# Kernel optimization log

Hardware: AMD Instinct MI355X
Metric: run time of the kernel (lower is better)

## Reference

```python
import jax, jax.numpy as jnp
import numpy as np

T, B, I, H, NCLS = 1024, 256, 128, 128, 18

def setup_inputs() -> dict:
    key = jax.random.key(0)
    ks = jax.random.split(key, 8)
    s = 1.0 / np.sqrt(H)  # torch nn.LSTM/Linear init bound
    inp = jax.random.normal(ks[0], (T, B, I), dtype=jnp.float32)
    hidden = jnp.zeros((1, B, H), dtype=jnp.float32)
    cell = jnp.zeros((1, B, H), dtype=jnp.float32)
    W_ih = jax.random.uniform(ks[1], (4 * H, I), jnp.float32, -s, s)
    W_hh = jax.random.uniform(ks[2], (4 * H, H), jnp.float32, -s, s)
    b_ih = jax.random.uniform(ks[3], (4 * H,), jnp.float32, -s, s)
    b_hh = jax.random.uniform(ks[4], (4 * H,), jnp.float32, -s, s)
    fc_W = jax.random.uniform(ks[5], (NCLS, H), jnp.float32, -s, s)
    fc_b = jax.random.uniform(ks[6], (NCLS,), jnp.float32, -s, s)
    return {"input": inp, "hidden": hidden, "cell": cell, "W_ih": W_ih,
            "W_hh": W_hh, "b_ih": b_ih, "b_hh": b_hh, "fc_W": fc_W, "fc_b": fc_b}

def reference(input, hidden, cell, W_ih, W_hh, b_ih, b_hh, fc_W, fc_b):
    # Single-layer unidirectional LSTM (PyTorch gate order i,f,g,o) + Linear head.
    h0, c0 = hidden[0], cell[0]  # [B,H]
    b = b_ih + b_hh

    def step(carry, x_t):
        h, c = carry
        gates = x_t @ W_ih.T + h @ W_hh.T + b  # [B,4H]
        i, f, g, o = jnp.split(gates, 4, axis=-1)
        i = jax.nn.sigmoid(i)
        f = jax.nn.sigmoid(f)
        g = jnp.tanh(g)
        o = jax.nn.sigmoid(o)
        c = f * c + i * g
        h = o * jnp.tanh(c)
        return (h, c), h

    (hT, cT), hs = jax.lax.scan(step, (h0, c0), input)  # hs: [T,B,H]
    out = hs @ fc_W.T + fc_b  # [T,B,18]
    return (out, (hT[None], cT[None]))
```

## Files before the change

### kernel.cpp

```cpp
#include <hip/hip_runtime.h>
#include <cstdint>
#include <cstddef>

#define TSTEPS 1024
#define NB 256
#define NI 128
#define NH 128
#define NC 18
#define CH 32
#define NCHUNK (TSTEPS/CH)
#define XGS 516

#define LOG2E_F     1.44269504088896f
#define TWO_LOG2E_F 2.88539008177793f

typedef _Float16 f16x8 __attribute__((ext_vector_type(8)));
typedef float    f32x4 __attribute__((ext_vector_type(4)));
typedef _Float16 half2_t __attribute__((ext_vector_type(2)));

__device__ __forceinline__ half2_t as_h2(uint32_t v){
  union { uint32_t u; half2_t h; } cv; cv.u = v; return cv.h;
}
__device__ __forceinline__ uint32_t pku(float a, float b){
  union { half2_t h; uint32_t u; } cv; cv.h.x=(_Float16)a; cv.h.y=(_Float16)b; return cv.u;
}
__device__ __forceinline__ float dot2f(half2_t a, half2_t b, float c){
#if __has_builtin(__builtin_amdgcn_fdot2)
  return __builtin_amdgcn_fdot2(a, b, c, false);
#else
  return c + (float)a.x*(float)b.x + (float)a.y*(float)b.y;
#endif
}
__device__ __forceinline__ float fast_rcp(float x){
#if __has_builtin(__builtin_amdgcn_rcpf)
  return __builtin_amdgcn_rcpf(x);
#else
  return 1.f / x;
#endif
}
__device__ __forceinline__ float exp2x(float v){
#if __has_builtin(__builtin_amdgcn_exp2f)
  return __builtin_amdgcn_exp2f(v);
#else
  return __expf(v * 0.6931471805599453f);
#endif
}
template<int CTRL>
__device__ __forceinline__ float qbcast(float v){
#if __has_builtin(__builtin_amdgcn_mov_dpp)
  union { float f; int i; } u; u.f = v;
  u.i = __builtin_amdgcn_mov_dpp(u.i, CTRL, 0xF, 0xF, false);
  return u.f;
#else
  return __shfl(v, ((threadIdx.x & 63) & ~3) + (CTRL & 3), 64);
#endif
}
__device__ __forceinline__ f16x8 ldrow_f16s(const float* base, float s){
  float4 f0 = ((const float4*)base)[0];
  float4 f1 = ((const float4*)base)[1];
  f16x8 r;
  r[0]=(_Float16)(f0.x*s); r[1]=(_Float16)(f0.y*s); r[2]=(_Float16)(f0.z*s); r[3]=(_Float16)(f0.w*s);
  r[4]=(_Float16)(f1.x*s); r[5]=(_Float16)(f1.y*s); r[6]=(_Float16)(f1.z*s); r[7]=(_Float16)(f1.w*s);
  return r;
}
__device__ __forceinline__ void barrier_lds(){
  asm volatile("s_waitcnt lgkmcnt(0)" ::: "memory");
  __builtin_amdgcn_s_barrier();
}

__global__ __launch_bounds__(512, 2) void lstm_mfma(
    const float* __restrict__ x,
    const float* __restrict__ h0,
    const float* __restrict__ c0,
    const float* __restrict__ Wih,
    const float* __restrict__ Whh,
    const float* __restrict__ bih,
    const float* __restrict__ bhh,
    const float* __restrict__ fcW,
    const float* __restrict__ fcb,
    float* __restrict__ out,
    float* __restrict__ hT,
    float* __restrict__ cT)
{
  const int b    = blockIdx.x;
  const int tid  = threadIdx.x;
  const int w    = tid >> 6;
  const int l    = tid & 63;
  const int n    = l & 15;
  const int quad = l >> 4;
  const int q4   = l & 3;
  const int c4   = (l >> 2) & 3;

  __shared__ __align__(16) _Float16 xs[CH][136];
  __shared__ __align__(16) float    xgp[CH][XGS];
  __shared__ __align__(16) _Float16 hist[CH][128];
  __shared__ __align__(16) uint32_t fcw[NC][66];

  const float sc = (q4 == 2) ? TWO_LOG2E_F : LOG2E_F;
  f16x8 whh[4][4], wih[4][4];
  float biasv[4];
#pragma unroll
  for (int m = 0; m < 4; ++m){
    const int row = q4*128 + w*16 + 4*m + c4;
#pragma unroll
    for (int kt = 0; kt < 4; ++kt){
      whh[m][kt] = ldrow_f16s(Whh + (size_t)row*NH + kt*32 + quad*8, sc);
      wih[m][kt] = ldrow_f16s(Wih + (size_t)row*NI + kt*32 + quad*8, sc);
    }
    biasv[m] = (bih[row] + bhh[row]) * sc;
  }

  const uint32_t smask = (q4 == 2) ? 0u : 0x80000000u;
  const float aK = (q4 == 2) ? 1.f : 0.f;
  const float sK = (q4 == 2) ? -2.f : 1.f;

  const int mycell = w*16 + quad*4 + c4;
  float cst = c0[(size_t)b*NH + mycell];
  float hlast = 0.f;

  if (tid < 128) hist[CH-1][tid] = (_Float16)h0[(size_t)b*NH + tid];
#pragma unroll
  for (int r = 0; r < 3; ++r){
    int idx = tid + 512*r;
    if (idx < NC*64){
      int j = idx >> 6, k = idx & 63;
      float2 f = ((const float2*)(fcW + (size_t)j*NH))[k];
      fcw[j][k] = pku(f.x, f.y);
    }
  }

  const int ttA = tid >> 5;
  const int ttB = ttA + 16;
  const int k4  = tid & 31;
  float4 xpA = ((const float4*)(x + ((size_t)ttA*NB + b)*NI))[k4];
  float4 xpB = ((const float4*)(x + ((size_t)ttB*NB + b)*NI))[k4];
  __syncthreads();

#pragma unroll 1
  for (int ck = 0; ck < NCHUNK; ++ck){
    const int t0 = ck*CH;

    {
      union { _Float16 h[4]; uint2 u2; } pa, pb;
      pa.h[0]=(_Float16)xpA.x; pa.h[1]=(_Float16)xpA.y;
      pa.h[2]=(_Float16)xpA.z; pa.h[3]=(_Float16)xpA.w;
      *(uint2*)&xs[ttA][4*k4] = pa.u2;
      pb.h[0]=(_Float16)xpB.x; pb.h[1]=(_Float16)xpB.y;
      pb.h[2]=(_Float16)xpB.z; pb.h[3]=(_Float16)xpB.w;
      *(uint2*)&xs[ttB][4*k4] = pb.u2;
    }
    barrier_lds();

    {
      f16x8 xa[2][4];
#pragma unroll
      for (int mt = 0; mt < 2; ++mt)
#pragma unroll
        for (int kt = 0; kt < 4; ++kt)
          xa[mt][kt] = *(const f16x8*)&xs[mt*16 + n][kt*32 + quad*8];

#pragma unroll
      for (int m = 0; m < 4; ++m){
#pragma unroll
        for (int mt = 0; mt < 2; ++mt){
          f32x4 acc = { biasv[m], biasv[m], biasv[m], biasv[m] };
#pragma unroll
          for (int kt = 0; kt < 4; ++kt)
            acc = __builtin_amdgcn_mfma_f32_16x16x32_f16(xa[mt][kt], wih[m][kt], acc, 0, 0, 0);
#pragma unroll
          for (int r = 0; r < 4; ++r)
            xgp[mt*16 + quad*4 + r][w*64 + n*4 + m] = acc[r];
        }
      }
    }

    if (ck + 1 < NCHUNK){
      const size_t t1 = (size_t)(t0 + CH);
      xpA = ((const float4*)(x + ((t1 + ttA)*NB + b)*NI))[k4];
      xpB = ((const float4*)(x + ((t1 + ttB)*NB + b)*NI))[k4];
    }
    barrier_lds();

#pragma unroll 4
    for (int tt = 0; tt < CH; ++tt){
      f32x4 sgv = *(const f32x4*)&xgp[tt][w*64 + n*4];
      const int rp = (tt + CH - 1) & (CH - 1);
      const _Float16* hprev = &hist[rp][0];
      f16x8 a0 = *(const f16x8*)&hprev[ 0 + quad*8];
      f16x8 a1 = *(const f16x8*)&hprev[32 + quad*8];
      f16x8 a2 = *(const f16x8*)&hprev[64 + quad*8];
      f16x8 a3 = *(const f16x8*)&hprev[96 + quad*8];
      float g0, g1, g2, g3;
      {
        f32x4 aA, aB;
        aA[0] = sgv[0];
        aA = __builtin_amdgcn_mfma_f32_16x16x32_f16(a0, whh[0][0], aA, 0, 0, 0);
        aA = __builtin_amdgcn_mfma_f32_16x16x32_f16(a1, whh[0][1], aA, 0, 0, 0);
        aB[0] = 0.f;
        aB = __builtin_amdgcn_mfma_f32_16x16x32_f16(a2, whh[0][2], aB, 0, 0, 0);
        aB = __builtin_amdgcn_mfma_f32_16x16x32_f16(a3, whh[0][3], aB, 0, 0, 0);
        g0 = aA[0] + aB[0];
      }
      {
        f32x4 aA, aB;
        aA[0] = sgv[1];
        aA = __builtin_amdgcn_mfma_f32_16x16x32_f16(a0, whh[1][0], aA, 0, 0, 0);
        aA = __builtin_amdgcn_mfma_f32_16x16x32_f16(a1, whh[1][1], aA, 0, 0, 0);
        aB[0] = 0.f;
        aB = __builtin_amdgcn_mfma_f32_16x16x32_f16(a2, whh[1][2], aB, 0, 0, 0);
        aB = __builtin_amdgcn_mfma_f32_16x16x32_f16(a3, whh[1][3], aB, 0, 0, 0);
        g1 = aA[0] + aB[0];
      }
      {
        f32x4 aA, aB;
        aA[0] = sgv[2];
        aA = __builtin_amdgcn_mfma_f32_16x16x32_f16(a0, whh[2][0], aA, 0, 0, 0);
        aA = __builtin_amdgcn_mfma_f32_16x16x32_f16(a1, whh[2][1], aA, 0, 0, 0);
        aB[0] = 0.f;
        aB = __builtin_amdgcn_mfma_f32_16x16x32_f16(a2, whh[2][2], aB, 0, 0, 0);
        aB = __builtin_amdgcn_mfma_f32_16x16x32_f16(a3, whh[2][3], aB, 0, 0, 0);
        g2 = aA[0] + aB[0];
      }
      {
        f32x4 aA, aB;
        aA[0] = sgv[3];
        aA = __builtin_amdgcn_mfma_f32_16x16x32_f16(a0, whh[3][0], aA, 0, 0, 0);
        aA = __builtin_amdgcn_mfma_f32_16x16x32_f16(a1, whh[3][1], aA, 0, 0, 0);
        aB[0] = 0.f;
        aB = __builtin_amdgcn_mfma_f32_16x16x32_f16(a2, whh[3][2], aB, 0, 0, 0);
        aB = __builtin_amdgcn_mfma_f32_16x16x32_f16(a3, whh[3][3], aB, 0, 0, 0);
        g3 = aA[0] + aB[0];
      }
      const bool qlo = (quad & 1) != 0;
      const bool qhi = (quad & 2) != 0;
      float gsel = qhi ? (qlo ? g3 : g2) : (qlo ? g1 : g0);
      union { float f; uint32_t u; } gx; gx.f = gsel; gx.u ^= smask;
      float ev  = exp2x(gx.f);
      float rr  = fast_rcp(1.f + ev);
      float act = __builtin_fmaf(sK, rr, aK);
      float vi = qbcast<0x00>(act);
      float vf = qbcast<0x55>(act);
      float vg = qbcast<0xAA>(act);
      float vo = qbcast<0xFF>(act);
      cst = __builtin_fmaf(vf, cst, vi*vg);
      float e2 = exp2x(cst * TWO_LOG2E_F);
      float tc = __builtin_fmaf(-2.f, fast_rcp(1.f + e2), 1.f);
      float hv = vo * tc;
      hlast = hv;
      if (q4 == 0)
        hist[tt][mycell] = (_Float16)hv;
      barrier_lds();
    }

    {
      const int tt = tid >> 4;
      const int jb = tid & 15;
      const uint4* hb = (const uint4*)&hist[tt][0];
#pragma unroll
      for (int jj = 0; jj < 2; ++jj){
        const int j = jj*16 + jb;
        if (j < NC){
          const uint2* fw = (const uint2*)&fcw[j][0];
          float a0=0.f, a1=0.f, a2=0.f, a3=0.f;
#pragma unroll
          for (int q = 0; q < 4; ++q){
            uint4 v0 = hb[q], v1 = hb[4+q], v2 = hb[8+q], v3 = hb[12+q];
            uint2 f0a = fw[2*q],    f0b = fw[2*q+1];
            uint2 f1a = fw[8+2*q],  f1b = fw[8+2*q+1];
            uint2 f2a = fw[16+2*q], f2b = fw[16+2*q+1];
            uint2 f3a = fw[24+2*q], f3b = fw[24+2*q+1];
            a0 = dot2f(as_h2(f0a.x), as_h2(v0.x), a0);
            a1 = dot2f(as_h2(f1a.x), as_h2(v1.x), a1);
            a2 = dot2f(as_h2(f2a.x), as_h2(v2.x), a2);
            a3 = dot2f(as_h2(f3a.x), as_h2(v3.x), a3);
            a0 = dot2f(as_h2(f0a.y), as_h2(v0.y), a0);
            a1 = dot2f(as_h2(f1a.y), as_h2(v1.y), a1);
            a2 = dot2f(as_h2(f2a.y), as_h2(v2.y), a2);
            a3 = dot2f(as_h2(f3a.y), as_h2(v3.y), a3);
            a0 = dot2f(as_h2(f0b.x), as_h2(v0.z), a0);
            a1 = dot2f(as_h2(f1b.x), as_h2(v1.z), a1);
            a2 = dot2f(as_h2(f2b.x), as_h2(v2.z), a2);
            a3 = dot2f(as_h2(f3b.x), as_h2(v3.z), a3);
            a0 = dot2f(as_h2(f0b.y), as_h2(v0.w), a0);
            a1 = dot2f(as_h2(f1b.y), as_h2(v1.w), a1);
            a2 = dot2f(as_h2(f2b.y), as_h2(v2.w), a2);
            a3 = dot2f(as_h2(f3b.y), as_h2(v3.w), a3);
          }
          out[(size_t)(t0+tt)*NB*NC + (size_t)b*NC + j] =
              (a0+a1) + (a2+a3) + fcb[j];
        }
      }
    }
  }

  if (q4 == 0){
    hT[(size_t)b*NH + mycell] = hlast;
    cT[(size_t)b*NH + mycell] = cst;
  }
}

extern "C" void kernel_launch(void* const* d_in, const int* in_sizes, int n_in,
                              void* d_out, int out_size, void* d_ws, size_t ws_size,
                              hipStream_t stream) {
  (void)in_sizes; (void)n_in; (void)d_ws; (void)ws_size; (void)out_size;
  const float* x   = (const float*)d_in[0];
  const float* h0  = (const float*)d_in[1];
  const float* c0  = (const float*)d_in[2];
  const float* Wih = (const float*)d_in[3];
  const float* Whh = (const float*)d_in[4];
  const float* bih = (const float*)d_in[5];
  const float* bhh = (const float*)d_in[6];
  const float* fcW = (const float*)d_in[7];
  const float* fcb = (const float*)d_in[8];
  float* out = (float*)d_out;
  float* hT  = out + (size_t)TSTEPS*NB*NC;
  float* cT  = hT + (size_t)NB*NH;
  hipLaunchKernelGGL(lstm_mfma, dim3(NB), dim3(512), 0, stream,
                     x, h0, c0, Wih, Whh, bih, bhh, fcW, fcb, out, hT, cT);
}
```

Before: 723.4 us.

## Halve LSTM block to 256 threads with two hidden cells per lane

The kernel now uses 4 waves of 256 threads instead of 8, and each wave owns 32 hidden cells instead of 16. Each lane therefore keeps twice as many W_hh/W_ih fragments in registers, issues 8 gate MFMA groups per step and updates two cells, with a packed half2 write into the history. The aim is cheaper per-timestep barriers and more MFMA work in flight per wave on the serial recurrence. In exchange register pressure doubles, which risks spills at one block per CU. The loader and FC-head work are remapped to fit the smaller block.

```diff
diff --git a/kernel.cpp b/kernel.cpp
--- a/kernel.cpp
+++ b/kernel.cpp
@@ -68,7 +68,7 @@
   __builtin_amdgcn_s_barrier();
 }
 
-__global__ __launch_bounds__(512, 2) void lstm_mfma(
+__global__ __launch_bounds__(256, 1) void lstm_mfma(
     const float* __restrict__ x,
     const float* __restrict__ h0,
     const float* __restrict__ c0,
@@ -97,11 +97,11 @@
   __shared__ __align__(16) uint32_t fcw[NC][66];
 
   const float sc = (q4 == 2) ? TWO_LOG2E_F : LOG2E_F;
-  f16x8 whh[4][4], wih[4][4];
-  float biasv[4];
-#pragma unroll
-  for (int m = 0; m < 4; ++m){
-    const int row = q4*128 + w*16 + 4*m + c4;
+  f16x8 whh[8][4], wih[8][4];
+  float biasv[8];
+#pragma unroll
+  for (int m = 0; m < 8; ++m){
+    const int row = q4*128 + w*32 + (m&3)*8 + (n>>2)*2 + (m>>2);
 #pragma unroll
     for (int kt = 0; kt < 4; ++kt){
       whh[m][kt] = ldrow_f16s(Whh + (size_t)row*NH + kt*32 + quad*8, sc);
@@ -114,14 +114,15 @@
   const float aK = (q4 == 2) ? 1.f : 0.f;
   const float sK = (q4 == 2) ? -2.f : 1.f;
 
-  const int mycell = w*16 + quad*4 + c4;
-  float cst = c0[(size_t)b*NH + mycell];
-  float hlast = 0.f;
+  const int cellA = w*32 + quad*8 + c4*2;
+  float cstA = c0[(size_t)b*NH + cellA];
+  float cstB = c0[(size_t)b*NH + cellA + 1];
+  float hlastA = 0.f, hlastB = 0.f;
 
   if (tid < 128) hist[CH-1][tid] = (_Float16)h0[(size_t)b*NH + tid];
 #pragma unroll
-  for (int r = 0; r < 3; ++r){
-    int idx = tid + 512*r;
+  for (int r = 0; r < 5; ++r){
+    int idx = tid + 256*r;
     if (idx < NC*64){
       int j = idx >> 6, k = idx & 63;
       float2 f = ((const float2*)(fcW + (size_t)j*NH))[k];
@@ -129,11 +130,18 @@
     }
   }
 
-  const int ttA = tid >> 5;
-  const int ttB = ttA + 16;
-  const int k4  = tid & 31;
-  float4 xpA = ((const float4*)(x + ((size_t)ttA*NB + b)*NI))[k4];
-  float4 xpB = ((const float4*)(x + ((size_t)ttB*NB + b)*NI))[k4];
+  const int hrow = tid >> 3;
+  const int hj   = tid & 7;
+  const float fj0 = fcb[hj];
+  const float fj1 = fcb[hj + 8];
+  const float fj2 = (hj < 2) ? fcb[16 + hj] : 0.f;
+
+  const int srow = tid >> 3;
+  const int sc8  = tid & 7;
+  float4 xp0 = ((const float4*)(x + ((size_t)srow*NB + b)*NI))[sc8];
+  float4 xp1 = ((const float4*)(x + ((size_t)srow*NB + b)*NI))[sc8 + 8];
+  float4 xp2 = ((const float4*)(x + ((size_t)srow*NB + b)*NI))[sc8 + 16];
+  float4 xp3 = ((const float4*)(x + ((size_t)srow*NB + b)*NI))[sc8 + 24];
   __syncthreads();
 
 #pragma unroll 1
@@ -141,13 +149,15 @@
     const int t0 = ck*CH;
 
     {
-      union { _Float16 h[4]; uint2 u2; } pa, pb;
-      pa.h[0]=(_Float16)xpA.x; pa.h[1]=(_Float16)xpA.y;
-      pa.h[2]=(_Float16)xpA.z; pa.h[3]=(_Float16)xpA.w;
-      *(uint2*)&xs[ttA][4*k4] = pa.u2;
-      pb.h[0]=(_Float16)xpB.x; pb.h[1]=(_Float16)xpB.y;
-      pb.h[2]=(_Float16)xpB.z; pb.h[3]=(_Float16)xpB.w;
-      *(uint2*)&xs[ttB][4*k4] = pb.u2;
+      union { _Float16 h[4]; uint2 u2; } p0, p1, p2, p3;
+      p0.h[0]=(_Float16)xp0.x; p0.h[1]=(_Float16)xp0.y; p0.h[2]=(_Float16)xp0.z; p0.h[3]=(_Float16)xp0.w;
+      p1.h[0]=(_Float16)xp1.x; p1.h[1]=(_Float16)xp1.y; p1.h[2]=(_Float16)xp1.z; p1.h[3]=(_Float16)xp1.w;
+      p2.h[0]=(_Float16)xp2.x; p2.h[1]=(_Float16)xp2.y; p2.h[2]=(_Float16)xp2.z; p2.h[3]=(_Float16)xp2.w;
+      p3.h[0]=(_Float16)xp3.x; p3.h[1]=(_Float16)xp3.y; p3.h[2]=(_Float16)xp3.z; p3.h[3]=(_Float16)xp3.w;
+      *(uint2*)&xs[srow][4*sc8]        = p0.u2;
+      *(uint2*)&xs[srow][4*(sc8 + 8)]  = p1.u2;
+      *(uint2*)&xs[srow][4*(sc8 + 16)] = p2.u2;
+      *(uint2*)&xs[srow][4*(sc8 + 24)] = p3.u2;
     }
     barrier_lds();
 
@@ -160,7 +170,7 @@
           xa[mt][kt] = *(const f16x8*)&xs[mt*16 + n][kt*32 + quad*8];
 
 #pragma unroll
-      for (int m = 0; m < 4; ++m){
+      for (int m = 0; m < 8; ++m){
 #pragma unroll
         for (int mt = 0; mt < 2; ++mt){
           f32x4 acc = { biasv[m], biasv[m], biasv[m], biasv[m] };
@@ -169,133 +179,106 @@
             acc = __builtin_amdgcn_mfma_f32_16x16x32_f16(xa[mt][kt], wih[m][kt], acc, 0, 0, 0);
 #pragma unroll
           for (int r = 0; r < 4; ++r)
-            xgp[mt*16 + quad*4 + r][w*64 + n*4 + m] = acc[r];
+            xgp[mt*16 + quad*4 + r][w*128 + n*8 + m] = acc[r];
         }
       }
     }
 
     if (ck + 1 < NCHUNK){
       const size_t t1 = (size_t)(t0 + CH);
-      xpA = ((const float4*)(x + ((t1 + ttA)*NB + b)*NI))[k4];
-      xpB = ((const float4*)(x + ((t1 + ttB)*NB + b)*NI))[k4];
+      xp0 = ((const float4*)(x + ((t1 + srow)*NB + b)*NI))[sc8];
+      xp1 = ((const float4*)(x + ((t1 + srow)*NB + b)*NI))[sc8 + 8];
+      xp2 = ((const float4*)(x + ((t1 + srow)*NB + b)*NI))[sc8 + 16];
+      xp3 = ((const float4*)(x + ((t1 + srow)*NB + b)*NI))[sc8 + 24];
     }
     barrier_lds();
 
-#pragma unroll 4
+#pragma unroll 2
     for (int tt = 0; tt < CH; ++tt){
-      f32x4 sgv = *(const f32x4*)&xgp[tt][w*64 + n*4];
+      f32x4 s0 = *(const f32x4*)&xgp[tt][w*128 + n*8];
+      f32x4 s1 = *(const f32x4*)&xgp[tt][w*128 + n*8 + 4];
       const int rp = (tt + CH - 1) & (CH - 1);
       const _Float16* hprev = &hist[rp][0];
       f16x8 a0 = *(const f16x8*)&hprev[ 0 + quad*8];
       f16x8 a1 = *(const f16x8*)&hprev[32 + quad*8];
       f16x8 a2 = *(const f16x8*)&hprev[64 + quad*8];
       f16x8 a3 = *(const f16x8*)&hprev[96 + quad*8];
-      float g0, g1, g2, g3;
-      {
+      float g[8];
+#pragma unroll
+      for (int m = 0; m < 4; ++m){
         f32x4 aA, aB;
-        aA[0] = sgv[0];
-        aA = __builtin_amdgcn_mfma_f32_16x16x32_f16(a0, whh[0][0], aA, 0, 0, 0);
-        aA = __builtin_amdgcn_mfma_f32_16x16x32_f16(a1, whh[0][1], aA, 0, 0, 0);
+        aA[0] = s0[m];
+        aA = __builtin_amdgcn_mfma_f32_16x16x32_f16(a0, whh[m][0], aA, 0, 0, 0);
+        aA = __builtin_amdgcn_mfma_f32_16x16x32_f16(a1, whh[m][1], aA, 0, 0, 0);
         aB[0] = 0.f;
-        aB = __builtin_amdgcn_mfma_f32_16x16x32_f16(a2, whh[0][2], aB, 0, 0, 0);
-        aB = __builtin_amdgcn_mfma_f32_16x16x32_f16(a3, whh[0][3], aB, 0, 0, 0);
-        g0 = aA[0] + aB[0];
+        aB = __builtin_amdgcn_mfma_f32_16x16x32_f16(a2, whh[m][2], aB, 0, 0, 0);
+        aB = __builtin_amdgcn_mfma_f32_16x16x32_f16(a3, whh[m][3], aB, 0, 0, 0);
+        g[m] = aA[0] + aB[0];
       }
-      {
+#pragma unroll
+      for (int m = 0; m < 4; ++m){
         f32x4 aA, aB;
-        aA[0] = sgv[1];
-        aA = __builtin_amdgcn_mfma_f32_16x16x32_f16(a0, whh[1][0], aA, 0, 0, 0);
-        aA = __builtin_amdgcn_mfma_f32_16x16x32_f16(a1, whh[1][1], aA, 0, 0, 0);
+        aA[0] = s1[m];
+        aA = __builtin_amdgcn_mfma_f32_16x16x32_f16(a0, whh[4+m][0], aA, 0, 0, 0);
+        aA = __builtin_amdgcn_mfma_f32_16x16x32_f16(a1, whh[4+m][1], aA, 0, 0, 0);
         aB[0] = 0.f;
-        aB = __builtin_amdgcn_mfma_f32_16x16x32_f16(a2, whh[1][2], aB, 0, 0, 0);
-        aB = __builtin_amdgcn_mfma_f32_16x16x32_f16(a3, whh[1][3], aB, 0, 0, 0);
-        g1 = aA[0] + aB[0];
-      }
-      {
-        f32x4 aA, aB;
-        aA[0] = sgv[2];
-        aA = __builtin_amdgcn_mfma_f32_16x16x32_f16(a0, whh[2][0], aA, 0, 0, 0);
-        aA = __builtin_amdgcn_mfma_f32_16x16x32_f16(a1, whh[2][1], aA, 0, 0, 0);
-        aB[0] = 0.f;
-        aB = __builtin_amdgcn_mfma_f32_16x16x32_f16(a2, whh[2][2], aB, 0, 0, 0);
-        aB = __builtin_amdgcn_mfma_f32_16x16x32_f16(a3, whh[2][3], aB, 0, 0, 0);
-        g2 = aA[0] + aB[0];
-      }
-      {
-        f32x4 aA, aB;
-        aA[0] = sgv[3];
-        aA = __builtin_amdgcn_mfma_f32_16x16x32_f16(a0, whh[3][0], aA, 0, 0, 0);
-        aA = __builtin_amdgcn_mfma_f32_16x16x32_f16(a1, whh[3][1], aA, 0, 0, 0);
-        aB[0] = 0.f;
-        aB = __builtin_amdgcn_mfma_f32_16x16x32_f16(a2, whh[3][2], aB, 0, 0, 0);
-        aB = __builtin_amdgcn_mfma_f32_16x16x32_f16(a3, whh[3][3], aB, 0, 0, 0);
-        g3 = aA[0] + aB[0];
+        aB = __builtin_amdgcn_mfma_f32_16x16x32_f16(a2, whh[4+m][2], aB, 0, 0, 0);
+        aB = __builtin_amdgcn_mfma_f32_16x16x32_f16(a3, whh[4+m][3], aB, 0, 0, 0);
+        g[4+m] = aA[0] + aB[0];
       }
       const bool qlo = (quad & 1) != 0;
       const bool qhi = (quad & 2) != 0;
-      float gsel = qhi ? (qlo ? g3 : g2) : (qlo ? g1 : g0);
-      union { float f; uint32_t u; } gx; gx.f = gsel; gx.u ^= smask;
-      float ev  = exp2x(gx.f);
-      float rr  = fast_rcp(1.f + ev);
-      float act = __builtin_fmaf(sK, rr, aK);
-      float vi = qbcast<0x00>(act);
-      float vf = qbcast<0x55>(act);
-      float vg = qbcast<0xAA>(act);
-      float vo = qbcast<0xFF>(act);
-      cst = __builtin_fmaf(vf, cst, vi*vg);
-      float e2 = exp2x(cst * TWO_LOG2E_F);
-      float tc = __builtin_fmaf(-2.f, fast_rcp(1.f + e2), 1.f);
-      float hv = vo * tc;
-      hlast = hv;
+      float gsA = qhi ? (qlo ? g[3] : g[2]) : (qlo ? g[1] : g[0]);
+      float gsB = qhi ? (qlo ? g[7] : g[6]) : (qlo ? g[5] : g[4]);
+      union { float f; uint32_t u; } ga, gb;
+      ga.f = gsA; ga.u ^= smask;
+      gb.f = gsB; gb.u ^= smask;
+      float actA = __builtin_fmaf(sK, fast_rcp(1.f + exp2x(ga.f)), aK);
+      float actB = __builtin_fmaf(sK, fast_rcp(1.f + exp2x(gb.f)), aK);
+      float viA = qbcast<0x00>(actA), vfA = qbcast<0x55>(actA);
+      float vgA = qbcast<0xAA>(actA), voA = qbcast<0xFF>(actA);
+      float viB = qbcast<0x00>(actB), vfB = qbcast<0x55>(actB);
+      float vgB = qbcast<0xAA>(actB), voB = qbcast<0xFF>(actB);
+      cstA = __builtin_fmaf(vfA, cstA, viA*vgA);
+      cstB = __builtin_fmaf(vfB, cstB, viB*vgB);
+      float tcA = __builtin_fmaf(-2.f, fast_rcp(1.f + exp2x(cstA * TWO_LOG2E_F)), 1.f);
+      float tcB = __builtin_fmaf(-2.f, fast_rcp(1.f + exp2x(cstB * TWO_LOG2E_F)), 1.f);
+      float hvA = voA * tcA;
+      float hvB = voB * tcB;
+      hlastA = hvA; hlastB = hvB;
       if (q4 == 0)
-        hist[tt][mycell] = (_Float16)hv;
+        *(uint32_t*)&hist[tt][cellA] = pku(hvA, hvB);
       barrier_lds();
     }
 
     {
-      const int tt = tid >> 4;
-      const int jb = tid & 15;
-      const uint4* hb = (const uint4*)&hist[tt][0];
-#pragma unroll
-      for (int jj = 0; jj < 2; ++jj){
-        const int j = jj*16 + jb;
-        if (j < NC){
+      const uint4* hb = (const uint4*)&hist[hrow][0];
+#pragma unroll
+      for (int jj = 0; jj < 3; ++jj){
+        const int j = (jj == 0) ? hj : (jj == 1) ? hj + 8 : 16 + hj;
+        const float fb0 = (jj == 0) ? fj0 : (jj == 1) ? fj1 : fj2;
+        if (jj < 2 || hj < 2){
           const uint2* fw = (const uint2*)&fcw[j][0];
           float a0=0.f, a1=0.f, a2=0.f, a3=0.f;
 #pragma unroll
-          for (int q = 0; q < 4; ++q){
-            uint4 v0 = hb[q], v1 = hb[4+q], v2 = hb[8+q], v3 = hb[12+q];
-            uint2 f0a = fw[2*q],    f0b = fw[2*q+1];
-            uint2 f1a = fw[8+2*q],  f1b = fw[8+2*q+1];
-            uint2 f2a = fw[16+2*q], f2b = fw[16+2*q+1];
-            uint2 f3a = fw[24+2*q], f3b = fw[24+2*q+1];
-            a0 = dot2f(as_h2(f0a.x), as_h2(v0.x), a0);
-            a1 = dot2f(as_h2(f1a.x), as_h2(v1.x), a1);
-            a2 = dot2f(as_h2(f2a.x), as_h2(v2.x), a2);
-            a3 = dot2f(as_h2(f3a.x), as_h2(v3.x), a3);
-            a0 = dot2f(as_h2(f0a.y), as_h2(v0.y), a0);
-            a1 = dot2f(as_h2(f1a.y), as_h2(v1.y), a1);
-            a2 = dot2f(as_h2(f2a.y), as_h2(v2.y), a2);
-            a3 = dot2f(as_h2(f3a.y), as_h2(v3.y), a3);
-            a0 = dot2f(as_h2(f0b.x), as_h2(v0.z), a0);
-            a1 = dot2f(as_h2(f1b.x), as_h2(v1.z), a1);
-            a2 = dot2f(as_h2(f2b.x), as_h2(v2.z), a2);
-            a3 = dot2f(as_h2(f3b.x), as_h2(v3.z), a3);
-            a0 = dot2f(as_h2(f0b.y), as_h2(v0.w), a0);
-            a1 = dot2f(as_h2(f1b.y), as_h2(v1.w), a1);
-            a2 = dot2f(as_h2(f2b.y), as_h2(v2.w), a2);
-            a3 = dot2f(as_h2(f3b.y), as_h2(v3.w), a3);
+          for (int k = 0; k < 16; ++k){
+            uint4 v = hb[k];
+            uint2 fa = fw[2*k], fb2 = fw[2*k+1];
+            a0 = dot2f(as_h2(fa.x),  as_h2(v.x), a0);
+            a1 = dot2f(as_h2(fa.y),  as_h2(v.y), a1);
+            a2 = dot2f(as_h2(fb2.x), as_h2(v.z), a2);
+            a3 = dot2f(as_h2(fb2.y), as_h2(v.w), a3);
           }
-          out[(size_t)(t0+tt)*NB*NC + (size_t)b*NC + j] =
-              (a0+a1) + (a2+a3) + fcb[j];
+          out[(size_t)(t0+hrow)*NB*NC + (size_t)b*NC + j] =
+              (a0+a1) + (a2+a3) + fb0;
         }
       }
     }
   }
 
   if (q4 == 0){
-    hT[(size_t)b*NH + mycell] = hlast;
-    cT[(size_t)b*NH + mycell] = cst;
+    *(float2*)&hT[(size_t)b*NH + cellA] = make_float2(hlastA, hlastB);
+    *(float2*)&cT[(size_t)b*NH + cellA] = make_float2(cstA, cstB);
   }
 }
 
@@ -315,6 +298,6 @@
   float* out = (float*)d_out;
   float* hT  = out + (size_t)TSTEPS*NB*NC;
   float* cT  = hT + (size_t)NB*NH;
-  hipLaunchKernelGGL(lstm_mfma, dim3(NB), dim3(512), 0, stream,
+  hipLaunchKernelGGL(lstm_mfma, dim3(NB), dim3(256), 0, stream,
                      x, h0, c0, Wih, Whh, bih, bhh, fcW, fcb, out, hT, cT);
 }
```

Result: slower. 923.7 us (+27.7%).

## Split each batch's LSTM recurrence across 16 wavefronts instead of 8

Applied to the files above, without the earlier changes.

Doubles the workgroup to 1024 threads, so each wave owns 8 hidden cells (2 gate-row tiles) instead of 16. This halves the serial MFMA chain per timestep on the recurrent critical path, at the cost of redundant activation lanes, a costlier 16-wave barrier each step, and one workgroup per CU instead of two. The FC head is also remapped to one output per thread, and the input staging now uses one load per thread.

```diff
diff --git a/kernel.cpp b/kernel.cpp
--- a/kernel.cpp
+++ b/kernel.cpp
@@ -68,7 +68,7 @@
   __builtin_amdgcn_s_barrier();
 }
 
-__global__ __launch_bounds__(512, 2) void lstm_mfma(
+__global__ __launch_bounds__(1024, 1) void lstm_mfma(
     const float* __restrict__ x,
     const float* __restrict__ h0,
     const float* __restrict__ c0,
@@ -90,6 +90,7 @@
   const int quad = l >> 4;
   const int q4   = l & 3;
   const int c4   = (l >> 2) & 3;
+  const int mg   = quad >> 1;
 
   __shared__ __align__(16) _Float16 xs[CH][136];
   __shared__ __align__(16) float    xgp[CH][XGS];
@@ -97,11 +98,11 @@
   __shared__ __align__(16) uint32_t fcw[NC][66];
 
   const float sc = (q4 == 2) ? TWO_LOG2E_F : LOG2E_F;
-  f16x8 whh[4][4], wih[4][4];
-  float biasv[4];
-#pragma unroll
-  for (int m = 0; m < 4; ++m){
-    const int row = q4*128 + w*16 + 4*m + c4;
+  f16x8 whh[2][4], wih[2][4];
+  float biasv[2];
+#pragma unroll
+  for (int m = 0; m < 2; ++m){
+    const int row = q4*128 + w*8 + m*4 + c4;
 #pragma unroll
     for (int kt = 0; kt < 4; ++kt){
       whh[m][kt] = ldrow_f16s(Whh + (size_t)row*NH + kt*32 + quad*8, sc);
@@ -114,14 +115,15 @@
   const float aK = (q4 == 2) ? 1.f : 0.f;
   const float sK = (q4 == 2) ? -2.f : 1.f;
 
-  const int mycell = w*16 + quad*4 + c4;
+  const int mycell = w*8 + mg*4 + c4;
   float cst = c0[(size_t)b*NH + mycell];
   float hlast = 0.f;
+  const bool writer = (q4 == 0) && ((quad & 1) == 0);
 
   if (tid < 128) hist[CH-1][tid] = (_Float16)h0[(size_t)b*NH + tid];
 #pragma unroll
-  for (int r = 0; r < 3; ++r){
-    int idx = tid + 512*r;
+  for (int r = 0; r < 2; ++r){
+    int idx = tid + 1024*r;
     if (idx < NC*64){
       int j = idx >> 6, k = idx & 63;
       float2 f = ((const float2*)(fcW + (size_t)j*NH))[k];
@@ -129,11 +131,13 @@
     }
   }
 
-  const int ttA = tid >> 5;
-  const int ttB = ttA + 16;
-  const int k4  = tid & 31;
-  float4 xpA = ((const float4*)(x + ((size_t)ttA*NB + b)*NI))[k4];
-  float4 xpB = ((const float4*)(x + ((size_t)ttB*NB + b)*NI))[k4];
+  const int hrow = tid >> 5;
+  const int hj   = tid & 31;
+  const float fjh = (hj < NC) ? fcb[hj] : 0.f;
+
+  const int srow = tid >> 5;
+  const int sc32 = tid & 31;
+  float4 xp = ((const float4*)(x + ((size_t)srow*NB + b)*NI))[sc32];
   __syncthreads();
 
 #pragma unroll 1
@@ -141,13 +145,10 @@
     const int t0 = ck*CH;
 
     {
-      union { _Float16 h[4]; uint2 u2; } pa, pb;
-      pa.h[0]=(_Float16)xpA.x; pa.h[1]=(_Float16)xpA.y;
-      pa.h[2]=(_Float16)xpA.z; pa.h[3]=(_Float16)xpA.w;
-      *(uint2*)&xs[ttA][4*k4] = pa.u2;
-      pb.h[0]=(_Float16)xpB.x; pb.h[1]=(_Float16)xpB.y;
-      pb.h[2]=(_Float16)xpB.z; pb.h[3]=(_Float16)xpB.w;
-      *(uint2*)&xs[ttB][4*k4] = pb.u2;
+      union { _Float16 h[4]; uint2 u2; } p;
+      p.h[0]=(_Float16)xp.x; p.h[1]=(_Float16)xp.y;
+      p.h[2]=(_Float16)xp.z; p.h[3]=(_Float16)xp.w;
+      *(uint2*)&xs[srow][4*sc32] = p.u2;
     }
     barrier_lds();
 
@@ -160,7 +161,7 @@
           xa[mt][kt] = *(const f16x8*)&xs[mt*16 + n][kt*32 + quad*8];
 
 #pragma unroll
-      for (int m = 0; m < 4; ++m){
+      for (int m = 0; m < 2; ++m){
 #pragma unroll
         for (int mt = 0; mt < 2; ++mt){
           f32x4 acc = { biasv[m], biasv[m], biasv[m], biasv[m] };
@@ -169,31 +170,30 @@
             acc = __builtin_amdgcn_mfma_f32_16x16x32_f16(xa[mt][kt], wih[m][kt], acc, 0, 0, 0);
 #pragma unroll
           for (int r = 0; r < 4; ++r)
-            xgp[mt*16 + quad*4 + r][w*64 + n*4 + m] = acc[r];
+            xgp[mt*16 + quad*4 + r][w*32 + n*2 + m] = acc[r];
         }
       }
     }
 
     if (ck + 1 < NCHUNK){
       const size_t t1 = (size_t)(t0 + CH);
-      xpA = ((const float4*)(x + ((t1 + ttA)*NB + b)*NI))[k4];
-      xpB = ((const float4*)(x + ((t1 + ttB)*NB + b)*NI))[k4];
+      xp = ((const float4*)(x + ((t1 + srow)*NB + b)*NI))[sc32];
     }
     barrier_lds();
 
-#pragma unroll 4
+#pragma unroll 2
     for (int tt = 0; tt < CH; ++tt){
-      f32x4 sgv = *(const f32x4*)&xgp[tt][w*64 + n*4];
+      float2 sg2 = *(const float2*)&xgp[tt][w*32 + n*2];
       const int rp = (tt + CH - 1) & (CH - 1);
       const _Float16* hprev = &hist[rp][0];
       f16x8 a0 = *(const f16x8*)&hprev[ 0 + quad*8];
       f16x8 a1 = *(const f16x8*)&hprev[32 + quad*8];
       f16x8 a2 = *(const f16x8*)&hprev[64 + quad*8];
       f16x8 a3 = *(const f16x8*)&hprev[96 + quad*8];
-      float g0, g1, g2, g3;
+      float g0, g1;
       {
         f32x4 aA, aB;
-        aA[0] = sgv[0];
+        aA[0] = sg2.x;
         aA = __builtin_amdgcn_mfma_f32_16x16x32_f16(a0, whh[0][0], aA, 0, 0, 0);
         aA = __builtin_amdgcn_mfma_f32_16x16x32_f16(a1, whh[0][1], aA, 0, 0, 0);
         aB[0] = 0.f;
@@ -203,7 +203,7 @@
       }
       {
         f32x4 aA, aB;
-        aA[0] = sgv[1];
+        aA[0] = sg2.y;
         aA = __builtin_amdgcn_mfma_f32_16x16x32_f16(a0, whh[1][0], aA, 0, 0, 0);
         aA = __builtin_amdgcn_mfma_f32_16x16x32_f16(a1, whh[1][1], aA, 0, 0, 0);
         aB[0] = 0.f;
@@ -211,89 +211,41 @@
         aB = __builtin_amdgcn_mfma_f32_16x16x32_f16(a3, whh[1][3], aB, 0, 0, 0);
         g1 = aA[0] + aB[0];
       }
-      {
-        f32x4 aA, aB;
-        aA[0] = sgv[2];
-        aA = __builtin_amdgcn_mfma_f32_16x16x32_f16(a0, whh[2][0], aA, 0, 0, 0);
-        aA = __builtin_amdgcn_mfma_f32_16x16x32_f16(a1, whh[2][1], aA, 0, 0, 0);
-        aB[0] = 0.f;
-        aB = __builtin_amdgcn_mfma_f32_16x16x32_f16(a2, whh[2][2], aB, 0, 0, 0);
-        aB = __builtin_amdgcn_mfma_f32_16x16x32_f16(a3, whh[2][3], aB, 0, 0, 0);
-        g2 = aA[0] + aB[0];
-      }
-      {
-        f32x4 aA, aB;
-        aA[0] = sgv[3];
-        aA = __builtin_amdgcn_mfma_f32_16x16x32_f16(a0, whh[3][0], aA, 0, 0, 0);
-        aA = __builtin_amdgcn_mfma_f32_16x16x32_f16(a1, whh[3][1], aA, 0, 0, 0);
-        aB[0] = 0.f;
-        aB = __builtin_amdgcn_mfma_f32_16x16x32_f16(a2, whh[3][2], aB, 0, 0, 0);
-        aB = __builtin_amdgcn_mfma_f32_16x16x32_f16(a3, whh[3][3], aB, 0, 0, 0);
-        g3 = aA[0] + aB[0];
-      }
-      const bool qlo = (quad & 1) != 0;
-      const bool qhi = (quad & 2) != 0;
-      float gsel = qhi ? (qlo ? g3 : g2) : (qlo ? g1 : g0);
+      float gsel = (quad & 2) ? g1 : g0;
       union { float f; uint32_t u; } gx; gx.f = gsel; gx.u ^= smask;
-      float ev  = exp2x(gx.f);
-      float rr  = fast_rcp(1.f + ev);
-      float act = __builtin_fmaf(sK, rr, aK);
+      float act = __builtin_fmaf(sK, fast_rcp(1.f + exp2x(gx.f)), aK);
       float vi = qbcast<0x00>(act);
       float vf = qbcast<0x55>(act);
       float vg = qbcast<0xAA>(act);
       float vo = qbcast<0xFF>(act);
       cst = __builtin_fmaf(vf, cst, vi*vg);
-      float e2 = exp2x(cst * TWO_LOG2E_F);
-      float tc = __builtin_fmaf(-2.f, fast_rcp(1.f + e2), 1.f);
+      float tc = __builtin_fmaf(-2.f, fast_rcp(1.f + exp2x(cst * TWO_LOG2E_F)), 1.f);
       float hv = vo * tc;
       hlast = hv;
-      if (q4 == 0)
+      if (writer)
         hist[tt][mycell] = (_Float16)hv;
       barrier_lds();
     }
 
-    {
-      const int tt = tid >> 4;
-      const int jb = tid & 15;
-      const uint4* hb = (const uint4*)&hist[tt][0];
-#pragma unroll
-      for (int jj = 0; jj < 2; ++jj){
-        const int j = jj*16 + jb;
-        if (j < NC){
-          const uint2* fw = (const uint2*)&fcw[j][0];
-          float a0=0.f, a1=0.f, a2=0.f, a3=0.f;
-#pragma unroll
-          for (int q = 0; q < 4; ++q){
-            uint4 v0 = hb[q], v1 = hb[4+q], v2 = hb[8+q], v3 = hb[12+q];
-            uint2 f0a = fw[2*q],    f0b = fw[2*q+1];
-            uint2 f1a = fw[8+2*q],  f1b = fw[8+2*q+1];
-            uint2 f2a = fw[16+2*q], f2b = fw[16+2*q+1];
-            uint2 f3a = fw[24+2*q], f3b = fw[24+2*q+1];
-            a0 = dot2f(as_h2(f0a.x), as_h2(v0.x), a0);
-            a1 = dot2f(as_h2(f1a.x), as_h2(v1.x), a1);
-            a2 = dot2f(as_h2(f2a.x), as_h2(v2.x), a2);
-            a3 = dot2f(as_h2(f3a.x), as_h2(v3.x), a3);
-            a0 = dot2f(as_h2(f0a.y), as_h2(v0.y), a0);
-            a1 = dot2f(as_h2(f1a.y), as_h2(v1.y), a1);
-            a2 = dot2f(as_h2(f2a.y), as_h2(v2.y), a2);
-            a3 = dot2f(as_h2(f3a.y), as_h2(v3.y), a3);
-            a0 = dot2f(as_h2(f0b.x), as_h2(v0.z), a0);
-            a1 = dot2f(as_h2(f1b.x), as_h2(v1.z), a1);
-            a2 = dot2f(as_h2(f2b.x), as_h2(v2.z), a2);
-            a3 = dot2f(as_h2(f3b.x), as_h2(v3.z), a3);
-            a0 = dot2f(as_h2(f0b.y), as_h2(v0.w), a0);
-            a1 = dot2f(as_h2(f1b.y), as_h2(v1.w), a1);
-            a2 = dot2f(as_h2(f2b.y), as_h2(v2.w), a2);
-            a3 = dot2f(as_h2(f3b.y), as_h2(v3.w), a3);
-          }
-          out[(size_t)(t0+tt)*NB*NC + (size_t)b*NC + j] =
-              (a0+a1) + (a2+a3) + fcb[j];
-        }
-      }
-    }
-  }
-
-  if (q4 == 0){
+    if (hj < NC){
+      const uint4* hb = (const uint4*)&hist[hrow][0];
+      const uint2* fw = (const uint2*)&fcw[hj][0];
+      float a0=0.f, a1=0.f, a2=0.f, a3=0.f;
+#pragma unroll
+      for (int k = 0; k < 16; ++k){
+        uint4 v = hb[k];
+        uint2 fa = fw[2*k], fb2 = fw[2*k+1];
+        a0 = dot2f(as_h2(fa.x),  as_h2(v.x), a0);
+        a1 = dot2f(as_h2(fa.y),  as_h2(v.y), a1);
+        a2 = dot2f(as_h2(fb2.x), as_h2(v.z), a2);
+        a3 = dot2f(as_h2(fb2.y), as_h2(v.w), a3);
+      }
+      out[(size_t)(t0+hrow)*NB*NC + (size_t)b*NC + hj] =
+          (a0+a1) + (a2+a3) + fjh;
+    }
+  }
+
+  if (writer){
     hT[(size_t)b*NH + mycell] = hlast;
     cT[(size_t)b*NH + mycell] = cst;
   }
@@ -315,6 +267,6 @@
   float* out = (float*)d_out;
   float* hT  = out + (size_t)TSTEPS*NB*NC;
   float* cT  = hT + (size_t)NB*NH;
-  hipLaunchKernelGGL(lstm_mfma, dim3(NB), dim3(512), 0, stream,
+  hipLaunchKernelGGL(lstm_mfma, dim3(NB), dim3(1024), 0, stream,
                      x, h0, c0, Wih, Whh, bih, bhh, fcW, fcb, out, hT, cT);
 }
```

After: 869.7 us. 20.2% more time.
